# Kernel optimization log

Measured on AMD Instinct MI355X. Metric: run time of the kernel, lower is better.

Reference implementation:

```python
import jax, jax.numpy as jnp
import numpy as np

ALPHA = 0.2  # LeakyReLU negative slope
NEG_INF = jnp.float32(-9e15)


def gat_layer(h, mask, W, a, concat):
    """Dense GAT layer (pyGAT style). h: [B,N,Fin], mask: [N,N] bool, W: [Fin,Fout], a: [2*Fout,1]."""
    Wh = h @ W                                   # [B,N,Fout]
    F_out = W.shape[-1]
    e_src = Wh @ a[:F_out]                       # [B,N,1]
    e_dst = Wh @ a[F_out:]                       # [B,N,1]
    e = jax.nn.leaky_relu(e_src + jnp.swapaxes(e_dst, -1, -2), ALPHA)  # [B,N,N]
    att = jnp.where(mask, e, NEG_INF)
    att = jax.nn.softmax(att, axis=-1)
    out = att @ Wh                               # [B,N,Fout]
    return jax.nn.elu(out) if concat else out


def setup_inputs() -> dict:
    key = jax.random.key(0)
    ks = jax.random.split(key, 8)
    B, N, nfeat, nhid, nheads, emb, nclass = 4, 2048, 128, 64, 8, 64, 16
    slices = jax.random.normal(ks[0], (B, N, nfeat), jnp.float32)
    adj = jax.random.randint(ks[1], (N, N), 0, 2, jnp.int32)
    s = 1.0 / float(np.sqrt(nfeat))
    Ws = jax.random.uniform(ks[2], (nheads, nfeat, nhid), jnp.float32, -s, s)
    As = jax.random.uniform(ks[3], (nheads, 2 * nhid, 1), jnp.float32, -s, s)
    W1 = jax.random.uniform(ks[4], (nhid * nheads, emb), jnp.float32, -s, s)
    a1 = jax.random.uniform(ks[5], (2 * emb, 1), jnp.float32, -s, s)
    W2 = jax.random.uniform(ks[6], (emb, nclass), jnp.float32, -s, s)
    a2 = jax.random.uniform(ks[7], (2 * nclass, 1), jnp.float32, -s, s)
    return {"slices": slices, "adj": adj, "Ws": Ws, "As": As,
            "W1": W1, "a1": a1, "W2": W2, "a2": a2}


def reference(slices, adj, Ws, As, W1, a1, W2, a2):
    # Eval mode: dropout = 0 (identity).
    mask = adj > 0                               # [N,N], broadcasts over batch
    # Multi-head GAT with concat=True (ELU inside each head), vectorized over heads.
    heads = jax.vmap(lambda W, a: gat_layer(slices, mask, W, a, True))(Ws, As)  # [H,B,N,nhid]
    H, B, N, nh = heads.shape
    x = jnp.moveaxis(heads, 0, 2).reshape(B, N, H * nh)  # concat along features, head-major
    image_feature = jax.nn.elu(gat_layer(x, mask, W1, a1, False))              # [B,N,emb]
    pre = jax.nn.elu(gat_layer(image_feature, mask, W2, a2, False))            # [B,N,nclass]
    pre = pre[:, 0, :]                                                         # [B,nclass]
    return image_feature, pre
```

## Files before the change

### kernel.cpp

```cpp
#include <hip/hip_runtime.h>
#include <hip/hip_bf16.h>
#include <cstdint>


#define NN 2048

typedef float f32x4 __attribute__((ext_vector_type(4)));
typedef __bf16 bf16x8 __attribute__((ext_vector_type(8)));
typedef _Float16 f16;
typedef _Float16 f16x8 __attribute__((ext_vector_type(8)));

__device__ __forceinline__ void gll16(const void* g, void* l) {
  __builtin_amdgcn_global_load_lds(
      (const __attribute__((address_space(1))) unsigned int*)g,
      (__attribute__((address_space(3))) unsigned int*)l, 16, 0, 0);
}

__global__ __launch_bounds__(256) void prep_k(
    const int* __restrict__ adj, unsigned char* __restrict__ pm,
    const float* __restrict__ Ws, __bf16* __restrict__ WsFh, __bf16* __restrict__ WsFl,
    const float* __restrict__ W1, __bf16* __restrict__ W1Fh, __bf16* __restrict__ W1Fl) {
  const int bx = blockIdx.x, t = threadIdx.x;
  if (bx < 2048) {
    const int i = bx;
#pragma unroll
    for (int jt = 0; jt < 8; ++jt) {
      const int j = jt * 256 + t;
      pm[((long)(j >> 5) << 16) + i * 32 + (j & 31)] =
          adj[(long)i * NN + j] > 0 ? 0xFFu : 0u;
    }
  } else if (bx < 2304) {
    const int idx = (bx - 2048) * 256 + t;
    const int inst = idx >> 13;
    const int rem = idx & 8191;
    const int k = rem >> 6, n = rem & 63;
    const float v = Ws[(long)inst * 8192 + rem];
    const __bf16 vh = (__bf16)v;
    const int pos = ((k >> 5) * 4 + (n >> 4)) * 512 + (((k >> 3) & 3) * 16 + (n & 15)) * 8 + (k & 7);
    WsFh[(long)inst * 8192 + pos] = vh;
    WsFl[(long)inst * 8192 + pos] = (__bf16)(v - (float)vh);
  } else {
    const int idx = (bx - 2304) * 256 + t;
    const int k = idx >> 6, n = idx & 63;
    const float v = W1[idx];
    const __bf16 vh = (__bf16)v;
    const int pos = ((k >> 5) * 4 + (n >> 4)) * 512 + (((k >> 3) & 3) * 16 + (n & 15)) * 8 + (k & 7);
    W1Fh[pos] = vh;
    W1Fl[pos] = (__bf16)(v - (float)vh);
  }
}

struct GemmLd {
  float4 a0, a1;
  bf16x8 bh[4], bl[4];
};

__global__ __launch_bounds__(128) void gemm_mfma_k(
    const float* __restrict__ Aall, const __bf16* __restrict__ WFhi,
    const __bf16* __restrict__ WFlo, const float* __restrict__ avecAll,
    f16* __restrict__ WhBAll, float* __restrict__ Eo, float* __restrict__ Go,
    f16* __restrict__ Fo, f16* __restrict__ Ho, float* __restrict__ pC,
    int K, int KS, long aStrideB) {
  const int p = blockIdx.y;
  const int ks = blockIdx.z;
  const float* A = Aall + (long)(p & 3) * aStrideB;
  const long wfOff = (long)(p >> 2) * K * 64;
  const bf16x8* BhF = (const bf16x8*)(WFhi + wfOff);
  const bf16x8* BlF = (const bf16x8*)(WFlo + wfOff);

  const int t = threadIdx.x, lane = t & 63, wave = t >> 6;
  const int quad = lane >> 4, lm = lane & 15;
  const int i0w = blockIdx.x * 32 + wave * 16;
  const float* Arow = A + (long)(i0w + lm) * K;
  const int kBeg = ks * (K / KS), kEnd = kBeg + K / KS;

  f32x4 acc[4];
#pragma unroll
  for (int nt = 0; nt < 4; ++nt) acc[nt] = (f32x4){0.f, 0.f, 0.f, 0.f};

  auto LOAD = [&](GemmLd& L, int k0) {
    L.a0 = *(const float4*)(Arow + k0 + quad * 8);
    L.a1 = *(const float4*)(Arow + k0 + quad * 8 + 4);
    const int bbase = (k0 >> 5) * 256 + lane;
#pragma unroll
    for (int nt = 0; nt < 4; ++nt) {
      L.bh[nt] = BhF[bbase + nt * 64];
      L.bl[nt] = BlF[bbase + nt * 64];
    }
  };
  auto STEP = [&](const GemmLd& L) {
    const float av8[8] = {L.a0.x, L.a0.y, L.a0.z, L.a0.w, L.a1.x, L.a1.y, L.a1.z, L.a1.w};
    bf16x8 ah, al;
#pragma unroll
    for (int j = 0; j < 8; ++j) {
      const __bf16 h = (__bf16)av8[j];
      ah[j] = h;
      al[j] = (__bf16)(av8[j] - (float)h);
    }
#pragma unroll
    for (int nt = 0; nt < 4; ++nt) {
      acc[nt] = __builtin_amdgcn_mfma_f32_16x16x32_bf16(ah, L.bh[nt], acc[nt], 0, 0, 0);
      acc[nt] = __builtin_amdgcn_mfma_f32_16x16x32_bf16(al, L.bh[nt], acc[nt], 0, 0, 0);
      acc[nt] = __builtin_amdgcn_mfma_f32_16x16x32_bf16(ah, L.bl[nt], acc[nt], 0, 0, 0);
    }
  };

  GemmLd La, Lb;
  LOAD(La, kBeg);
  for (int k0 = kBeg; k0 < kEnd; k0 += 64) {
    LOAD(Lb, k0 + 32);
    STEP(La);
    LOAD(La, (k0 + 64 < kEnd) ? k0 + 64 : kBeg);
    STEP(Lb);
  }

  if (KS > 1) {
    float* pc = pC + ((long)(p * KS + ks) * NN) * 64;
#pragma unroll
    for (int reg = 0; reg < 4; ++reg) {
      const int row = i0w + quad * 4 + reg;
#pragma unroll
      for (int nt = 0; nt < 4; ++nt) pc[(long)row * 64 + nt * 16 + lm] = acc[nt][reg];
    }
    return;
  }

  const float* av = avecAll + (long)(p >> 2) * 128;
  f16* WhB = WhBAll + (long)p * NN * 64;
  float* E = Eo + (long)p * NN;
  float* G = Go + (long)p * NN;
  f16* F = Fo + (long)p * NN;
  f16* Hh = Ho + (long)p * NN;

  float alo[4], ahi[4];
#pragma unroll
  for (int nt = 0; nt < 4; ++nt) {
    alo[nt] = av[nt * 16 + lm];
    ahi[nt] = av[64 + nt * 16 + lm];
  }
#pragma unroll
  for (int reg = 0; reg < 4; ++reg) {
    float es = 0.f, ed = 0.f;
#pragma unroll
    for (int nt = 0; nt < 4; ++nt) {
      es += acc[nt][reg] * alo[nt];
      ed += acc[nt][reg] * ahi[nt];
    }
#pragma unroll
    for (int m = 1; m < 16; m <<= 1) {
      es += __shfl_xor(es, m);
      ed += __shfl_xor(ed, m);
    }
    if (lm == 0) {
      const int r = i0w + quad * 4 + reg;
      E[r] = __expf(es);
      G[r] = __expf(0.2f * es);
      F[r] = (f16)__expf(ed);
      Hh[r] = (f16)__expf(0.2f * ed);
    }
  }

  const int r0 = i0w + quad * 4;
  const long base = ((long)(r0 >> 5) * 4) * 512 + (((r0 >> 3) & 3) * 16 + lm) * 8 + (r0 & 7);
#pragma unroll
  for (int nt = 0; nt < 4; ++nt) {
    union { f16 h[4]; uint2 u; } pk;
#pragma unroll
    for (int q = 0; q < 4; ++q) pk.h[q] = (f16)acc[nt][q];
    *(uint2*)(WhB + base + nt * 512) = pk.u;
  }
}

__global__ __launch_bounds__(256) void gemm_epi_k(
    const float* __restrict__ pC, const float* __restrict__ avec,
    f16* __restrict__ WhBAll, float* __restrict__ Eo, float* __restrict__ Go,
    f16* __restrict__ Fo, f16* __restrict__ Ho, int KS) {
  const int inst = blockIdx.y;
  const int t = threadIdx.x;
  const int row = blockIdx.x * 16 + (t >> 4);
  const int cg = t & 15;
  f32x4 c = (f32x4){0.f, 0.f, 0.f, 0.f};
  for (int ks = 0; ks < KS; ++ks)
    c += *(const f32x4*)(pC + (((long)(inst * KS + ks) * NN) + row) * 64 + cg * 4);
  float es = 0.f, ed = 0.f;
#pragma unroll
  for (int q = 0; q < 4; ++q) {
    const int n = cg * 4 + q;
    es += c[q] * avec[n];
    ed += c[q] * avec[64 + n];
  }
#pragma unroll
  for (int m = 1; m < 16; m <<= 1) {
    es += __shfl_xor(es, m);
    ed += __shfl_xor(ed, m);
  }
  if (cg == 0) {
    Eo[(long)inst * NN + row] = __expf(es);
    Go[(long)inst * NN + row] = __expf(0.2f * es);
    Fo[(long)inst * NN + row] = (f16)__expf(ed);
    Ho[(long)inst * NN + row] = (f16)__expf(0.2f * ed);
  }
  f16* WhB = WhBAll + (long)inst * NN * 64;
#pragma unroll
  for (int q = 0; q < 4; ++q) {
    const int n = cg * 4 + q;
    const int pos = ((row >> 5) * 4 + (n >> 4)) * 512 + (((row >> 3) & 3) * 16 + (n & 15)) * 8 + (row & 7);
    WhB[pos] = (f16)c[q];
  }
}

__global__ __launch_bounds__(512) void attn_k(
    const f16* __restrict__ WhBAll, const float* __restrict__ Eb,
    const float* __restrict__ Gb, const f16* __restrict__ Fb,
    const f16* __restrict__ Hb, const unsigned char* __restrict__ pm,
    float* __restrict__ out1, int rowStride, long strideB,
    int jsCount, float* __restrict__ partAcc, float* __restrict__ partSum) {
  const int p = blockIdx.z;
  const int js = blockIdx.y;
  const f16* WhB = WhBAll + (long)p * NN * 64;
  const float* E = Eb + (long)p * NN;
  const float* G = Gb + (long)p * NN;
  const f16* F = Fb + (long)p * NN;
  const f16* Hv = Hb + (long)p * NN;
  const int t = threadIdx.x, lane = t & 63, wave = t >> 6;
  const int rw = wave & 3, half = wave >> 2;
  const int quad = lane >> 4, lm = lane & 15;
  const int i0 = blockIdx.x * 128;
  const int rbase = rw * 32;
  const int span = 64 / jsCount;
  const int nIter = span / 2;
  const int nStep = nIter / 2;
  const int kbBeg = js * span + half * nIter;

  __shared__ __align__(16) char pool[40960];
  f16* Fs = (f16*)pool;
  f16* Hs = (f16*)(pool + 4096);
  char* ring = pool + 8192 + half * 16384;

  const int r0g = i0 + rbase + lm, r1g = i0 + rbase + 16 + lm;
  const f16 e0 = (f16)E[r0g], g0 = (f16)G[r0g];
  const f16 e1 = (f16)E[r1g], g1 = (f16)G[r1g];
  f16x8 e0v, g0v, e1v, g1v;
#pragma unroll
  for (int j = 0; j < 8; ++j) { e0v[j] = e0; g0v[j] = g0; e1v[j] = e1; g1v[j] = g1; }

  f16x8 ones;
#pragma unroll
  for (int j = 0; j < 8; ++j) ones[j] = (lm == 0) ? (f16)1.0f : (f16)0.0f;

  if (wave == 0) {
#pragma unroll
    for (int c = 0; c < 4; ++c) gll16((const char*)F + c * 1024 + lane * 16, pool + c * 1024);
  } else if (wave == 1) {
#pragma unroll
    for (int c = 0; c < 4; ++c) gll16((const char*)Hv + c * 1024 + lane * 16, pool + 4096 + c * 1024);
  }
  if (rw == 0) {
    const char* gB = (const char*)WhB + (long)kbBeg * 4096;
#pragma unroll
    for (int c = 0; c < 8; ++c) gll16(gB + c * 1024 + lane * 16, ring + c * 1024);
  }
  __syncthreads();

  f32x4 acc0[4], acc1[4], sum0, sum1;
#pragma unroll
  for (int nt = 0; nt < 4; ++nt) {
    acc0[nt] = (f32x4){0.f, 0.f, 0.f, 0.f};
    acc1[nt] = (f32x4){0.f, 0.f, 0.f, 0.f};
  }
  sum0 = (f32x4){0.f, 0.f, 0.f, 0.f};
  sum1 = (f32x4){0.f, 0.f, 0.f, 0.f};

  const unsigned char* mp0 = pm + (long)(i0 + rbase + lm) * 32 + quad * 8;
  const unsigned char* mp1 = pm + (long)(i0 + rbase + 16 + lm) * 32 + quad * 8;

  for (int s = 0; s < nStep; ++s) {
    if (rw == 0 && s + 1 < nStep) {
      char* dst = ring + ((s + 1) & 1) * 8192;
      const char* gB = (const char*)WhB + (long)(kbBeg + (s + 1) * 2) * 4096;
#pragma unroll
      for (int c = 0; c < 8; ++c) gll16(gB + c * 1024 + lane * 16, dst + c * 1024);
    }
    const char* slot = ring + (s & 1) * 8192;
#pragma unroll
    for (int u = 0; u < 2; ++u) {
      const int kb = kbBeg + s * 2 + u;
      const char* bt = slot + u * 4096;
      const uint2 m0 = *(const uint2*)(mp0 + ((long)kb << 16));
      const uint2 m1 = *(const uint2*)(mp1 + ((long)kb << 16));
      const f16x8 F8 = *(const f16x8*)(Fs + kb * 32 + quad * 8);
      const f16x8 H8 = *(const f16x8*)(Hs + kb * 32 + quad * 8);

      union { f16x8 v; uint4 u4; } A0, A1;
      A0.v = __builtin_elementwise_max(e0v * F8, g0v * H8);
      A1.v = __builtin_elementwise_max(e1v * F8, g1v * H8);
      A0.u4.x &= __builtin_amdgcn_perm(0u, m0.x, 0x01010000u);
      A0.u4.y &= __builtin_amdgcn_perm(0u, m0.x, 0x03030202u);
      A0.u4.z &= __builtin_amdgcn_perm(0u, m0.y, 0x01010000u);
      A0.u4.w &= __builtin_amdgcn_perm(0u, m0.y, 0x03030202u);
      A1.u4.x &= __builtin_amdgcn_perm(0u, m1.x, 0x01010000u);
      A1.u4.y &= __builtin_amdgcn_perm(0u, m1.x, 0x03030202u);
      A1.u4.z &= __builtin_amdgcn_perm(0u, m1.y, 0x01010000u);
      A1.u4.w &= __builtin_amdgcn_perm(0u, m1.y, 0x03030202u);

#pragma unroll
      for (int nt = 0; nt < 4; ++nt) {
        const f16x8 bfr = *(const f16x8*)(bt + (nt * 64 + lane) * 16);
        acc0[nt] = __builtin_amdgcn_mfma_f32_16x16x32_f16(A0.v, bfr, acc0[nt], 0, 0, 0);
        acc1[nt] = __builtin_amdgcn_mfma_f32_16x16x32_f16(A1.v, bfr, acc1[nt], 0, 0, 0);
      }
      sum0 = __builtin_amdgcn_mfma_f32_16x16x32_f16(A0.v, ones, sum0, 0, 0, 0);
      sum1 = __builtin_amdgcn_mfma_f32_16x16x32_f16(A1.v, ones, sum1, 0, 0, 0);
    }
    __syncthreads();
  }

  float* cmb = (float*)pool;
  if (half == 1) {
    float* dst = &cmb[(rw * 64 + lane) * 40];
#pragma unroll
    for (int nt = 0; nt < 4; ++nt) {
      *(f32x4*)(dst + nt * 4) = acc0[nt];
      *(f32x4*)(dst + 16 + nt * 4) = acc1[nt];
    }
    *(f32x4*)(dst + 32) = sum0;
    *(f32x4*)(dst + 36) = sum1;
  }
  __syncthreads();
  if (half == 1) return;
  {
    const float* src = &cmb[(rw * 64 + lane) * 40];
#pragma unroll
    for (int nt = 0; nt < 4; ++nt) {
      acc0[nt] += *(const f32x4*)(src + nt * 4);
      acc1[nt] += *(const f32x4*)(src + 16 + nt * 4);
    }
    sum0 += *(const f32x4*)(src + 32);
    sum1 += *(const f32x4*)(src + 36);
  }

  if (jsCount == 1) {
#pragma unroll
    for (int g = 0; g < 2; ++g) {
      const f32x4* acc = g ? acc1 : acc0;
      const f32x4 sm = g ? sum1 : sum0;
#pragma unroll
      for (int reg = 0; reg < 4; ++reg) {
        const int row = i0 + rbase + g * 16 + quad * 4 + reg;
        const float ls = __shfl(sm[reg], quad * 16);
        const float il = ls > 0.f ? 1.f / ls : 0.f;
#pragma unroll
        for (int nt = 0; nt < 4; ++nt) {
          float v = acc[nt][reg] * il;
          v = v > 0.f ? v : expm1f(v);
          const long o = (long)(p & 3) * strideB + (long)row * rowStride + (p >> 2) * 64 + nt * 16 + lm;
          out1[o] = v;
        }
      }
    }
  } else {
    float* pAcc = partAcc + ((long)p * jsCount + js) * NN * 64;
    float* pSum = partSum + ((long)p * jsCount + js) * NN;
#pragma unroll
    for (int g = 0; g < 2; ++g) {
      const f32x4* acc = g ? acc1 : acc0;
      const f32x4 sm = g ? sum1 : sum0;
#pragma unroll
      for (int reg = 0; reg < 4; ++reg) {
        const int row = i0 + rbase + g * 16 + quad * 4 + reg;
#pragma unroll
        for (int nt = 0; nt < 4; ++nt) pAcc[(long)row * 64 + nt * 16 + lm] = acc[nt][reg];
        if (lm == 0) pSum[row] = sm[reg];
      }
    }
  }
}

__global__ __launch_bounds__(256) void combine_k(const float* __restrict__ partAcc,
                                                 const float* __restrict__ partSum,
                                                 float* __restrict__ img,
                                                 float* __restrict__ out, int JS) {
  const long idx = (long)blockIdx.x * 256 + threadIdx.x;
  const int cg = idx & 15;
  const int row = (int)((idx >> 4) & (NN - 1));
  const int inst = (int)(idx >> 15);
  f32x4 v = (f32x4){0.f, 0.f, 0.f, 0.f};
  float s = 0.f;
  for (int js = 0; js < JS; ++js) {
    const long b = ((long)inst * JS + js) * NN;
    v += *(const f32x4*)(partAcc + (b + row) * 64 + cg * 4);
    s += partSum[b + row];
  }
  const float il = s > 0.f ? 1.f / s : 0.f;
  f32x4 r;
#pragma unroll
  for (int q = 0; q < 4; ++q) {
    float x = v[q] * il;
    r[q] = x > 0.f ? x : expm1f(x);
  }
  const long o = ((long)inst * NN + row) * 64 + cg * 4;
  *(f32x4*)(img + o) = r;
  *(f32x4*)(out + o) = r;
}

__global__ __launch_bounds__(256) void layer3a_k(
    const float* __restrict__ img, const float* __restrict__ W2,
    const float* __restrict__ a2, const unsigned char* __restrict__ pm,
    float* __restrict__ pOut ) {
  const int bb = blockIdx.x, chunk = blockIdx.y, t = threadIdx.x;
  const float* A = img + (long)bb * NN * 64;
  __shared__ float w2alo[64], w2ahi[64];
  __shared__ float W2s[64][17];
  __shared__ float redc[4][17];
  if (t < 64) {
    float sl = 0.f, sh = 0.f;
#pragma unroll
    for (int c = 0; c < 16; ++c) {
      const float wv = W2[t * 16 + c];
      W2s[t][c] = wv;
      sl += wv * a2[c];
      sh += wv * a2[16 + c];
    }
    w2alo[t] = sl;
    w2ahi[t] = sh;
  }
  __syncthreads();

  float es = 0.f;
#pragma unroll 16
  for (int k = 0; k < 64; ++k) es += A[k] * w2alo[k];

  const int j = chunk * 256 + t;
  float arow[64];
#pragma unroll
  for (int q = 0; q < 16; ++q) *(f32x4*)(arow + q * 4) = *(const f32x4*)(A + (long)j * 64 + q * 4);
  float ed = 0.f;
#pragma unroll
  for (int k = 0; k < 64; ++k) ed += arow[k] * w2ahi[k];
  float e = es + ed;
  e = fmaxf(e, 0.2f * e);
  const float pv = pm[((long)(j >> 5) << 16) + (j & 31)] ? __expf(e) : 0.f;

  float acc[16];
#pragma unroll
  for (int c = 0; c < 16; ++c) {
    float wh = 0.f;
#pragma unroll
    for (int k = 0; k < 64; ++k) wh += arow[k] * W2s[k][c];
    acc[c] = pv * wh;
  }
  float lsum = pv;

#pragma unroll
  for (int off = 32; off > 0; off >>= 1) {
    lsum += __shfl_down(lsum, off);
#pragma unroll
    for (int c = 0; c < 16; ++c) acc[c] += __shfl_down(acc[c], off);
  }
  if ((t & 63) == 0) {
    const int wv = t >> 6;
#pragma unroll
    for (int c = 0; c < 16; ++c) redc[wv][c] = acc[c];
    redc[wv][16] = lsum;
  }
  __syncthreads();
  if (t < 17) {
    pOut[((long)bb * 8 + chunk) * 17 + t] =
        redc[0][t] + redc[1][t] + redc[2][t] + redc[3][t];
  }
}

__global__ __launch_bounds__(64) void layer3b_k(const float* __restrict__ pOut,
                                                float* __restrict__ outPre) {
  const int t = threadIdx.x;
  if (t >= 64) return;
  const int bb = t >> 4, c = t & 15;
  float a = 0.f, l = 0.f;
#pragma unroll
  for (int ch = 0; ch < 8; ++ch) {
    a += pOut[((long)bb * 8 + ch) * 17 + c];
    l += pOut[((long)bb * 8 + ch) * 17 + 16];
  }
  float v = a / l;
  v = v > 0.f ? v : expm1f(v);
  outPre[bb * 16 + c] = v;
}

extern "C" void kernel_launch(void* const* d_in, const int* in_sizes, int n_in,
                              void* d_out, int out_size, void* d_ws, size_t ws_size,
                              hipStream_t stream) {
  (void)in_sizes; (void)n_in; (void)out_size; (void)ws_size;
  constexpr int B = 4, N = NN, JS2 = 4, KS2 = 4;

  const float* slices = (const float*)d_in[0];
  const int* adj = (const int*)d_in[1];
  const float* Ws = (const float*)d_in[2];
  const float* As = (const float*)d_in[3];
  const float* W1 = (const float*)d_in[4];
  const float* a1 = (const float*)d_in[5];
  const float* W2 = (const float*)d_in[6];
  const float* a2 = (const float*)d_in[7];
  float* out = (float*)d_out;

  char* w = (char*)d_ws;
  size_t off = 0;
  auto alloc = [&](size_t bytes) {
    void* ptr = w + off;
    off += (bytes + 255) & ~(size_t)255;
    return ptr;
  };
  unsigned char* pm = (unsigned char*)alloc((size_t)64 * 65536);
  __bf16* WsFh = (__bf16*)alloc((size_t)8 * 128 * 64 * 2);
  __bf16* WsFl = (__bf16*)alloc((size_t)8 * 128 * 64 * 2);
  __bf16* W1Fh = (__bf16*)alloc((size_t)512 * 64 * 2);
  __bf16* W1Fl = (__bf16*)alloc((size_t)512 * 64 * 2);
  f16* WhB1 = (f16*)alloc((size_t)32 * N * 64 * 2);
  float* E1 = (float*)alloc((size_t)32 * N * 4);
  float* G1 = (float*)alloc((size_t)32 * N * 4);
  f16* F1 = (f16*)alloc((size_t)32 * N * 2);
  f16* H1 = (f16*)alloc((size_t)32 * N * 2);
  float* x = (float*)alloc((size_t)B * N * 512 * 4);
  float* pC2 = (float*)alloc((size_t)B * KS2 * N * 64 * 4);
  f16* WhB2 = (f16*)alloc((size_t)B * N * 64 * 2);
  float* E2 = (float*)alloc((size_t)B * N * 4);
  float* G2 = (float*)alloc((size_t)B * N * 4);
  f16* F2 = (f16*)alloc((size_t)B * N * 2);
  f16* H2 = (f16*)alloc((size_t)B * N * 2);
  float* img = (float*)alloc((size_t)B * N * 64 * 4);
  float* pAcc2 = (float*)alloc((size_t)B * JS2 * N * 64 * 4);
  float* pSum2 = (float*)alloc((size_t)B * JS2 * N * 4);
  float* pL3 = (float*)alloc((size_t)B * 8 * 17 * 4);

  prep_k<<<dim3(2432), dim3(256), 0, stream>>>(adj, pm, Ws, WsFh, WsFl, W1, W1Fh, W1Fl);

  gemm_mfma_k<<<dim3(N / 32, 32, 1), dim3(128), 0, stream>>>(
      slices, WsFh, WsFl, As, WhB1, E1, G1, F1, H1, (float*)nullptr,
      128, 1, (long)N * 128);
  attn_k<<<dim3(N / 128, 1, 32), dim3(512), 0, stream>>>(
      WhB1, E1, G1, F1, H1, pm, x, 512, (long)N * 512,
      1, (float*)nullptr, (float*)nullptr);

  gemm_mfma_k<<<dim3(N / 32, 4, KS2), dim3(128), 0, stream>>>(
      x, W1Fh, W1Fl, a1, (f16*)nullptr, (float*)nullptr, (float*)nullptr,
      (f16*)nullptr, (f16*)nullptr, pC2, 512, KS2, (long)N * 512);
  gemm_epi_k<<<dim3(N / 16, 4), dim3(256), 0, stream>>>(
      pC2, a1, WhB2, E2, G2, F2, H2, KS2);
  attn_k<<<dim3(N / 128, JS2, 4), dim3(512), 0, stream>>>(
      WhB2, E2, G2, F2, H2, pm, (float*)nullptr, 64, (long)N * 64,
      JS2, pAcc2, pSum2);
  combine_k<<<dim3(B * N * 16 / 256), dim3(256), 0, stream>>>(pAcc2, pSum2, img, out, JS2);

  layer3a_k<<<dim3(B, 8), dim3(256), 0, stream>>>(img, W2, a2, pm, pL3);
  layer3b_k<<<dim3(1), dim3(64), 0, stream>>>(pL3, out + (size_t)B * N * 64);
}
```

Before: 162.3 us.

## Fuse split-K GEMM reduction, enlarge attention tiles, merge layer-3 kernels via ticket

The second-layer split-K GEMM and its separate epilogue kernel are replaced by a single 512-thread kernel that reduces the four K slices in shared memory. The attention kernel now gives each wave 64 rows instead of 32 and drops the LDS ring and global_load_lds staging in favour of direct register double-buffered loads. The two layer-3 kernels are merged using an atomic ticket, so the last block does the final combine. The aim is fewer launches and less global round-trip traffic, at the cost of more register pressure in attention and the loss of LDS sharing of B tiles.

```diff
diff --git a/kernel.cpp b/kernel.cpp
--- a/kernel.cpp
+++ b/kernel.cpp
@@ -10,17 +10,13 @@
 typedef _Float16 f16;
 typedef _Float16 f16x8 __attribute__((ext_vector_type(8)));
 
-__device__ __forceinline__ void gll16(const void* g, void* l) {
-  __builtin_amdgcn_global_load_lds(
-      (const __attribute__((address_space(1))) unsigned int*)g,
-      (__attribute__((address_space(3))) unsigned int*)l, 16, 0, 0);
-}
-
 __global__ __launch_bounds__(256) void prep_k(
     const int* __restrict__ adj, unsigned char* __restrict__ pm,
     const float* __restrict__ Ws, __bf16* __restrict__ WsFh, __bf16* __restrict__ WsFl,
-    const float* __restrict__ W1, __bf16* __restrict__ W1Fh, __bf16* __restrict__ W1Fl) {
+    const float* __restrict__ W1, __bf16* __restrict__ W1Fh, __bf16* __restrict__ W1Fl,
+    unsigned int* __restrict__ ticket) {
   const int bx = blockIdx.x, t = threadIdx.x;
+  if (bx == 0 && t == 0) *ticket = 0u;
   if (bx < 2048) {
     const int i = bx;
 #pragma unroll
@@ -59,10 +55,9 @@
     const float* __restrict__ Aall, const __bf16* __restrict__ WFhi,
     const __bf16* __restrict__ WFlo, const float* __restrict__ avecAll,
     f16* __restrict__ WhBAll, float* __restrict__ Eo, float* __restrict__ Go,
-    f16* __restrict__ Fo, f16* __restrict__ Ho, float* __restrict__ pC,
-    int K, int KS, long aStrideB) {
+    f16* __restrict__ Fo, f16* __restrict__ Ho,
+    int K, long aStrideB) {
   const int p = blockIdx.y;
-  const int ks = blockIdx.z;
   const float* A = Aall + (long)(p & 3) * aStrideB;
   const long wfOff = (long)(p >> 2) * K * 64;
   const bf16x8* BhF = (const bf16x8*)(WFhi + wfOff);
@@ -72,7 +67,7 @@
   const int quad = lane >> 4, lm = lane & 15;
   const int i0w = blockIdx.x * 32 + wave * 16;
   const float* Arow = A + (long)(i0w + lm) * K;
-  const int kBeg = ks * (K / KS), kEnd = kBeg + K / KS;
+  const int kBeg = 0, kEnd = K;
 
   f32x4 acc[4];
 #pragma unroll
@@ -114,17 +109,6 @@
     STEP(Lb);
   }
 
-  if (KS > 1) {
-    float* pc = pC + ((long)(p * KS + ks) * NN) * 64;
-#pragma unroll
-    for (int reg = 0; reg < 4; ++reg) {
-      const int row = i0w + quad * 4 + reg;
-#pragma unroll
-      for (int nt = 0; nt < 4; ++nt) pc[(long)row * 64 + nt * 16 + lm] = acc[nt][reg];
-    }
-    return;
-  }
-
   const float* av = avecAll + (long)(p >> 2) * 128;
   f16* WhB = WhBAll + (long)p * NN * 64;
   float* E = Eo + (long)p * NN;
@@ -171,43 +155,110 @@
   }
 }
 
-__global__ __launch_bounds__(256) void gemm_epi_k(
-    const float* __restrict__ pC, const float* __restrict__ avec,
+__global__ __launch_bounds__(512) void gemm2_k(
+    const float* __restrict__ Aall, const __bf16* __restrict__ WFhi,
+    const __bf16* __restrict__ WFlo, const float* __restrict__ avec,
     f16* __restrict__ WhBAll, float* __restrict__ Eo, float* __restrict__ Go,
-    f16* __restrict__ Fo, f16* __restrict__ Ho, int KS) {
-  const int inst = blockIdx.y;
-  const int t = threadIdx.x;
-  const int row = blockIdx.x * 16 + (t >> 4);
-  const int cg = t & 15;
-  f32x4 c = (f32x4){0.f, 0.f, 0.f, 0.f};
-  for (int ks = 0; ks < KS; ++ks)
-    c += *(const f32x4*)(pC + (((long)(inst * KS + ks) * NN) + row) * 64 + cg * 4);
-  float es = 0.f, ed = 0.f;
-#pragma unroll
-  for (int q = 0; q < 4; ++q) {
-    const int n = cg * 4 + q;
-    es += c[q] * avec[n];
-    ed += c[q] * avec[64 + n];
-  }
-#pragma unroll
-  for (int m = 1; m < 16; m <<= 1) {
-    es += __shfl_xor(es, m);
-    ed += __shfl_xor(ed, m);
-  }
-  if (cg == 0) {
-    Eo[(long)inst * NN + row] = __expf(es);
-    Go[(long)inst * NN + row] = __expf(0.2f * es);
-    Fo[(long)inst * NN + row] = (f16)__expf(ed);
-    Ho[(long)inst * NN + row] = (f16)__expf(0.2f * ed);
-  }
-  f16* WhB = WhBAll + (long)inst * NN * 64;
-#pragma unroll
-  for (int q = 0; q < 4; ++q) {
-    const int n = cg * 4 + q;
-    const int pos = ((row >> 5) * 4 + (n >> 4)) * 512 + (((row >> 3) & 3) * 16 + (n & 15)) * 8 + (row & 7);
-    WhB[pos] = (f16)c[q];
-  }
-}
+    f16* __restrict__ Fo, f16* __restrict__ Ho) {
+  const int p = blockIdx.y;
+  const float* A = Aall + (long)p * NN * 512;
+  const bf16x8* BhF = (const bf16x8*)WFhi;
+  const bf16x8* BlF = (const bf16x8*)WFlo;
+  const int t = threadIdx.x, lane = t & 63, wave = t >> 6;
+  const int ks = wave & 3, rh = wave >> 2;
+  const int quad = lane >> 4, lm = lane & 15;
+  const int i0 = blockIdx.x * 32;
+  const float* Arow = A + (long)(i0 + rh * 16 + lm) * 512;
+  const int kBeg = ks * 128, kEnd = kBeg + 128;
+
+  f32x4 acc[4];
+#pragma unroll
+  for (int nt = 0; nt < 4; ++nt) acc[nt] = (f32x4){0.f, 0.f, 0.f, 0.f};
+
+  auto LOAD = [&](GemmLd& L, int k0) {
+    L.a0 = *(const float4*)(Arow + k0 + quad * 8);
+    L.a1 = *(const float4*)(Arow + k0 + quad * 8 + 4);
+    const int bbase = (k0 >> 5) * 256 + lane;
+#pragma unroll
+    for (int nt = 0; nt < 4; ++nt) {
+      L.bh[nt] = BhF[bbase + nt * 64];
+      L.bl[nt] = BlF[bbase + nt * 64];
+    }
+  };
+  auto STEP = [&](const GemmLd& L) {
+    const float av8[8] = {L.a0.x, L.a0.y, L.a0.z, L.a0.w, L.a1.x, L.a1.y, L.a1.z, L.a1.w};
+    bf16x8 ah, al;
+#pragma unroll
+    for (int j = 0; j < 8; ++j) {
+      const __bf16 h = (__bf16)av8[j];
+      ah[j] = h;
+      al[j] = (__bf16)(av8[j] - (float)h);
+    }
+#pragma unroll
+    for (int nt = 0; nt < 4; ++nt) {
+      acc[nt] = __builtin_amdgcn_mfma_f32_16x16x32_bf16(ah, L.bh[nt], acc[nt], 0, 0, 0);
+      acc[nt] = __builtin_amdgcn_mfma_f32_16x16x32_bf16(al, L.bh[nt], acc[nt], 0, 0, 0);
+      acc[nt] = __builtin_amdgcn_mfma_f32_16x16x32_bf16(ah, L.bl[nt], acc[nt], 0, 0, 0);
+    }
+  };
+
+  GemmLd La, Lb;
+  LOAD(La, kBeg);
+  for (int k0 = kBeg; k0 < kEnd; k0 += 64) {
+    LOAD(Lb, k0 + 32);
+    STEP(La);
+    LOAD(La, (k0 + 64 < kEnd) ? k0 + 64 : kBeg);
+    STEP(Lb);
+  }
+
+  __shared__ __align__(16) float red[8][4][64][4];
+#pragma unroll
+  for (int nt = 0; nt < 4; ++nt) *(f32x4*)&red[wave][nt][lane][0] = acc[nt];
+  __syncthreads();
+
+  const int n = lane, rgrp = wave;
+  const int rh2 = rgrp >> 2, q2 = rgrp & 3;
+  const int ln = q2 * 16 + (n & 15), ntq = n >> 4;
+  f32x4 c4 = *(const f32x4*)&red[rh2 * 4 + 0][ntq][ln][0];
+#pragma unroll
+  for (int ksum = 1; ksum < 4; ++ksum)
+    c4 += *(const f32x4*)&red[rh2 * 4 + ksum][ntq][ln][0];
+
+  f32x4 es4 = c4 * avec[n];
+  f32x4 ed4 = c4 * avec[64 + n];
+#pragma unroll
+  for (int m = 1; m < 64; m <<= 1) {
+#pragma unroll
+    for (int q = 0; q < 4; ++q) {
+      es4[q] += __shfl_xor(es4[q], m);
+      ed4[q] += __shfl_xor(ed4[q], m);
+    }
+  }
+  const int row0 = i0 + rgrp * 4;
+  if (n == 0) {
+#pragma unroll
+    for (int reg = 0; reg < 4; ++reg) {
+      const int row = row0 + reg;
+      Eo[(long)p * NN + row] = __expf(es4[reg]);
+      Go[(long)p * NN + row] = __expf(0.2f * es4[reg]);
+      Fo[(long)p * NN + row] = (f16)__expf(ed4[reg]);
+      Ho[(long)p * NN + row] = (f16)__expf(0.2f * ed4[reg]);
+    }
+  }
+  f16* WhB = WhBAll + (long)p * NN * 64;
+  union { f16 h[4]; uint2 u; } pk;
+#pragma unroll
+  for (int reg = 0; reg < 4; ++reg) pk.h[reg] = (f16)c4[reg];
+  const long pos = ((long)(row0 >> 5) * 4 + ntq) * 512 +
+                   ((((row0 >> 3) & 3) * 16 + (n & 15)) * 8) + (row0 & 7);
+  *(uint2*)(WhB + pos) = pk.u;
+}
+
+struct KbLd {
+  f16x8 F8, H8;
+  f16x8 b[4];
+  uint2 m[4];
+};
 
 __global__ __launch_bounds__(512) void attn_k(
     const f16* __restrict__ WhBAll, const float* __restrict__ Eb,
@@ -220,138 +271,115 @@
   const f16* WhB = WhBAll + (long)p * NN * 64;
   const float* E = Eb + (long)p * NN;
   const float* G = Gb + (long)p * NN;
-  const f16* F = Fb + (long)p * NN;
-  const f16* Hv = Hb + (long)p * NN;
+  const f16* Fg = Fb + (long)p * NN;
+  const f16* Hg = Hb + (long)p * NN;
   const int t = threadIdx.x, lane = t & 63, wave = t >> 6;
   const int rw = wave & 3, half = wave >> 2;
   const int quad = lane >> 4, lm = lane & 15;
-  const int i0 = blockIdx.x * 128;
-  const int rbase = rw * 32;
+  const int i0 = blockIdx.x * 256;
+  const int rbase = rw * 64;
   const int span = 64 / jsCount;
   const int nIter = span / 2;
-  const int nStep = nIter / 2;
-  const int kbBeg = js * span + half * nIter;
-
-  __shared__ __align__(16) char pool[40960];
-  f16* Fs = (f16*)pool;
-  f16* Hs = (f16*)(pool + 4096);
-  char* ring = pool + 8192 + half * 16384;
-
-  const int r0g = i0 + rbase + lm, r1g = i0 + rbase + 16 + lm;
-  const f16 e0 = (f16)E[r0g], g0 = (f16)G[r0g];
-  const f16 e1 = (f16)E[r1g], g1 = (f16)G[r1g];
-  f16x8 e0v, g0v, e1v, g1v;
-#pragma unroll
-  for (int j = 0; j < 8; ++j) { e0v[j] = e0; g0v[j] = g0; e1v[j] = e1; g1v[j] = g1; }
+  const int kbBeg = js * span + half * nIter, kbEnd = kbBeg + nIter;
+
+  __shared__ __align__(16) float cmb[20480];
+
+  f16x8 ev[4], gv[4];
+#pragma unroll
+  for (int g = 0; g < 4; ++g) {
+    const int r = i0 + rbase + g * 16 + lm;
+    const f16 e = (f16)E[r], gg = (f16)G[r];
+#pragma unroll
+    for (int j = 0; j < 8; ++j) { ev[g][j] = e; gv[g][j] = gg; }
+  }
 
   f16x8 ones;
 #pragma unroll
   for (int j = 0; j < 8; ++j) ones[j] = (lm == 0) ? (f16)1.0f : (f16)0.0f;
 
-  if (wave == 0) {
-#pragma unroll
-    for (int c = 0; c < 4; ++c) gll16((const char*)F + c * 1024 + lane * 16, pool + c * 1024);
-  } else if (wave == 1) {
-#pragma unroll
-    for (int c = 0; c < 4; ++c) gll16((const char*)Hv + c * 1024 + lane * 16, pool + 4096 + c * 1024);
-  }
-  if (rw == 0) {
-    const char* gB = (const char*)WhB + (long)kbBeg * 4096;
-#pragma unroll
-    for (int c = 0; c < 8; ++c) gll16(gB + c * 1024 + lane * 16, ring + c * 1024);
-  }
-  __syncthreads();
-
-  f32x4 acc0[4], acc1[4], sum0, sum1;
-#pragma unroll
-  for (int nt = 0; nt < 4; ++nt) {
-    acc0[nt] = (f32x4){0.f, 0.f, 0.f, 0.f};
-    acc1[nt] = (f32x4){0.f, 0.f, 0.f, 0.f};
-  }
-  sum0 = (f32x4){0.f, 0.f, 0.f, 0.f};
-  sum1 = (f32x4){0.f, 0.f, 0.f, 0.f};
-
-  const unsigned char* mp0 = pm + (long)(i0 + rbase + lm) * 32 + quad * 8;
-  const unsigned char* mp1 = pm + (long)(i0 + rbase + 16 + lm) * 32 + quad * 8;
-
-  for (int s = 0; s < nStep; ++s) {
-    if (rw == 0 && s + 1 < nStep) {
-      char* dst = ring + ((s + 1) & 1) * 8192;
-      const char* gB = (const char*)WhB + (long)(kbBeg + (s + 1) * 2) * 4096;
-#pragma unroll
-      for (int c = 0; c < 8; ++c) gll16(gB + c * 1024 + lane * 16, dst + c * 1024);
-    }
-    const char* slot = ring + (s & 1) * 8192;
-#pragma unroll
-    for (int u = 0; u < 2; ++u) {
-      const int kb = kbBeg + s * 2 + u;
-      const char* bt = slot + u * 4096;
-      const uint2 m0 = *(const uint2*)(mp0 + ((long)kb << 16));
-      const uint2 m1 = *(const uint2*)(mp1 + ((long)kb << 16));
-      const f16x8 F8 = *(const f16x8*)(Fs + kb * 32 + quad * 8);
-      const f16x8 H8 = *(const f16x8*)(Hs + kb * 32 + quad * 8);
-
-      union { f16x8 v; uint4 u4; } A0, A1;
-      A0.v = __builtin_elementwise_max(e0v * F8, g0v * H8);
-      A1.v = __builtin_elementwise_max(e1v * F8, g1v * H8);
-      A0.u4.x &= __builtin_amdgcn_perm(0u, m0.x, 0x01010000u);
-      A0.u4.y &= __builtin_amdgcn_perm(0u, m0.x, 0x03030202u);
-      A0.u4.z &= __builtin_amdgcn_perm(0u, m0.y, 0x01010000u);
-      A0.u4.w &= __builtin_amdgcn_perm(0u, m0.y, 0x03030202u);
-      A1.u4.x &= __builtin_amdgcn_perm(0u, m1.x, 0x01010000u);
-      A1.u4.y &= __builtin_amdgcn_perm(0u, m1.x, 0x03030202u);
-      A1.u4.z &= __builtin_amdgcn_perm(0u, m1.y, 0x01010000u);
-      A1.u4.w &= __builtin_amdgcn_perm(0u, m1.y, 0x03030202u);
-
-#pragma unroll
-      for (int nt = 0; nt < 4; ++nt) {
-        const f16x8 bfr = *(const f16x8*)(bt + (nt * 64 + lane) * 16);
-        acc0[nt] = __builtin_amdgcn_mfma_f32_16x16x32_f16(A0.v, bfr, acc0[nt], 0, 0, 0);
-        acc1[nt] = __builtin_amdgcn_mfma_f32_16x16x32_f16(A1.v, bfr, acc1[nt], 0, 0, 0);
-      }
-      sum0 = __builtin_amdgcn_mfma_f32_16x16x32_f16(A0.v, ones, sum0, 0, 0, 0);
-      sum1 = __builtin_amdgcn_mfma_f32_16x16x32_f16(A1.v, ones, sum1, 0, 0, 0);
-    }
-    __syncthreads();
-  }
-
-  float* cmb = (float*)pool;
+  f32x4 acc[4][4], sum[4];
+#pragma unroll
+  for (int g = 0; g < 4; ++g) {
+    sum[g] = (f32x4){0.f, 0.f, 0.f, 0.f};
+#pragma unroll
+    for (int nt = 0; nt < 4; ++nt) acc[g][nt] = (f32x4){0.f, 0.f, 0.f, 0.f};
+  }
+
+  const unsigned char* mp[4];
+#pragma unroll
+  for (int g = 0; g < 4; ++g)
+    mp[g] = pm + (long)(i0 + rbase + g * 16 + lm) * 32 + quad * 8;
+
+  auto LD = [&](KbLd& L, int kb) {
+    L.F8 = *(const f16x8*)(Fg + kb * 32 + quad * 8);
+    L.H8 = *(const f16x8*)(Hg + kb * 32 + quad * 8);
+#pragma unroll
+    for (int nt = 0; nt < 4; ++nt)
+      L.b[nt] = *(const f16x8*)(WhB + (long)kb * 2048 + (nt * 64 + lane) * 8);
+#pragma unroll
+    for (int g = 0; g < 4; ++g)
+      L.m[g] = *(const uint2*)(mp[g] + ((long)kb << 16));
+  };
+  auto CP = [&](const KbLd& L) {
+    union { f16x8 v; uint4 u4; } A[4];
+#pragma unroll
+    for (int g = 0; g < 4; ++g) {
+      A[g].v = __builtin_elementwise_max(ev[g] * L.F8, gv[g] * L.H8);
+      A[g].u4.x &= __builtin_amdgcn_perm(0u, L.m[g].x, 0x01010000u);
+      A[g].u4.y &= __builtin_amdgcn_perm(0u, L.m[g].x, 0x03030202u);
+      A[g].u4.z &= __builtin_amdgcn_perm(0u, L.m[g].y, 0x01010000u);
+      A[g].u4.w &= __builtin_amdgcn_perm(0u, L.m[g].y, 0x03030202u);
+    }
+#pragma unroll
+    for (int nt = 0; nt < 4; ++nt) {
+#pragma unroll
+      for (int g = 0; g < 4; ++g)
+        acc[g][nt] = __builtin_amdgcn_mfma_f32_16x16x32_f16(A[g].v, L.b[nt], acc[g][nt], 0, 0, 0);
+    }
+#pragma unroll
+    for (int g = 0; g < 4; ++g)
+      sum[g] = __builtin_amdgcn_mfma_f32_16x16x32_f16(A[g].v, ones, sum[g], 0, 0, 0);
+  };
+
+  KbLd La, Lb2;
+  LD(La, kbBeg);
+  for (int kb = kbBeg; kb < kbEnd; kb += 2) {
+    LD(Lb2, kb + 1);
+    CP(La);
+    if (kb + 2 < kbEnd) LD(La, kb + 2);
+    CP(Lb2);
+  }
+
   if (half == 1) {
-    float* dst = &cmb[(rw * 64 + lane) * 40];
-#pragma unroll
-    for (int nt = 0; nt < 4; ++nt) {
-      *(f32x4*)(dst + nt * 4) = acc0[nt];
-      *(f32x4*)(dst + 16 + nt * 4) = acc1[nt];
-    }
-    *(f32x4*)(dst + 32) = sum0;
-    *(f32x4*)(dst + 36) = sum1;
+#pragma unroll
+    for (int g = 0; g < 4; ++g) {
+#pragma unroll
+      for (int nt = 0; nt < 4; ++nt)
+        *(f32x4*)&cmb[((rw * 20 + g * 4 + nt) * 64 + lane) * 4] = acc[g][nt];
+      *(f32x4*)&cmb[((rw * 20 + 16 + g) * 64 + lane) * 4] = sum[g];
+    }
   }
   __syncthreads();
   if (half == 1) return;
-  {
-    const float* src = &cmb[(rw * 64 + lane) * 40];
-#pragma unroll
-    for (int nt = 0; nt < 4; ++nt) {
-      acc0[nt] += *(const f32x4*)(src + nt * 4);
-      acc1[nt] += *(const f32x4*)(src + 16 + nt * 4);
-    }
-    sum0 += *(const f32x4*)(src + 32);
-    sum1 += *(const f32x4*)(src + 36);
+#pragma unroll
+  for (int g = 0; g < 4; ++g) {
+#pragma unroll
+    for (int nt = 0; nt < 4; ++nt)
+      acc[g][nt] += *(const f32x4*)&cmb[((rw * 20 + g * 4 + nt) * 64 + lane) * 4];
+    sum[g] += *(const f32x4*)&cmb[((rw * 20 + 16 + g) * 64 + lane) * 4];
   }
 
   if (jsCount == 1) {
 #pragma unroll
-    for (int g = 0; g < 2; ++g) {
-      const f32x4* acc = g ? acc1 : acc0;
-      const f32x4 sm = g ? sum1 : sum0;
+    for (int g = 0; g < 4; ++g) {
 #pragma unroll
       for (int reg = 0; reg < 4; ++reg) {
         const int row = i0 + rbase + g * 16 + quad * 4 + reg;
-        const float ls = __shfl(sm[reg], quad * 16);
+        const float ls = __shfl(sum[g][reg], quad * 16);
         const float il = ls > 0.f ? 1.f / ls : 0.f;
 #pragma unroll
         for (int nt = 0; nt < 4; ++nt) {
-          float v = acc[nt][reg] * il;
+          float v = acc[g][nt][reg] * il;
           v = v > 0.f ? v : expm1f(v);
           const long o = (long)(p & 3) * strideB + (long)row * rowStride + (p >> 2) * 64 + nt * 16 + lm;
           out1[o] = v;
@@ -362,15 +390,13 @@
     float* pAcc = partAcc + ((long)p * jsCount + js) * NN * 64;
     float* pSum = partSum + ((long)p * jsCount + js) * NN;
 #pragma unroll
-    for (int g = 0; g < 2; ++g) {
-      const f32x4* acc = g ? acc1 : acc0;
-      const f32x4 sm = g ? sum1 : sum0;
+    for (int g = 0; g < 4; ++g) {
 #pragma unroll
       for (int reg = 0; reg < 4; ++reg) {
         const int row = i0 + rbase + g * 16 + quad * 4 + reg;
 #pragma unroll
-        for (int nt = 0; nt < 4; ++nt) pAcc[(long)row * 64 + nt * 16 + lm] = acc[nt][reg];
-        if (lm == 0) pSum[row] = sm[reg];
+        for (int nt = 0; nt < 4; ++nt) pAcc[(long)row * 64 + nt * 16 + lm] = acc[g][nt][reg];
+        if (lm == 0) pSum[row] = sum[g][reg];
       }
     }
   }
@@ -406,12 +432,14 @@
 __global__ __launch_bounds__(256) void layer3a_k(
     const float* __restrict__ img, const float* __restrict__ W2,
     const float* __restrict__ a2, const unsigned char* __restrict__ pm,
-    float* __restrict__ pOut ) {
+    float* __restrict__ pOut , float* __restrict__ outPre,
+    unsigned int* __restrict__ ticket) {
   const int bb = blockIdx.x, chunk = blockIdx.y, t = threadIdx.x;
   const float* A = img + (long)bb * NN * 64;
   __shared__ float w2alo[64], w2ahi[64];
   __shared__ float W2s[64][17];
   __shared__ float redc[4][17];
+  __shared__ int lastS;
   if (t < 64) {
     float sl = 0.f, sh = 0.f;
 #pragma unroll
@@ -465,32 +493,36 @@
   }
   __syncthreads();
   if (t < 17) {
-    pOut[((long)bb * 8 + chunk) * 17 + t] =
-        redc[0][t] + redc[1][t] + redc[2][t] + redc[3][t];
-  }
-}
-
-__global__ __launch_bounds__(64) void layer3b_k(const float* __restrict__ pOut,
-                                                float* __restrict__ outPre) {
-  const int t = threadIdx.x;
-  if (t >= 64) return;
-  const int bb = t >> 4, c = t & 15;
-  float a = 0.f, l = 0.f;
-#pragma unroll
-  for (int ch = 0; ch < 8; ++ch) {
-    a += pOut[((long)bb * 8 + ch) * 17 + c];
-    l += pOut[((long)bb * 8 + ch) * 17 + 16];
-  }
-  float v = a / l;
-  v = v > 0.f ? v : expm1f(v);
-  outPre[bb * 16 + c] = v;
+    __hip_atomic_store(&pOut[((long)bb * 8 + chunk) * 17 + t],
+                       redc[0][t] + redc[1][t] + redc[2][t] + redc[3][t],
+                       __ATOMIC_RELAXED, __HIP_MEMORY_SCOPE_AGENT);
+  }
+  __syncthreads();
+  if (t == 0)
+    lastS = (__hip_atomic_fetch_add(ticket, 1u, __ATOMIC_ACQ_REL,
+                                    __HIP_MEMORY_SCOPE_AGENT) == 31u);
+  __syncthreads();
+  if (lastS && t < 64) {
+    const int b2 = t >> 4, c2 = t & 15;
+    float a = 0.f, l = 0.f;
+#pragma unroll
+    for (int ch = 0; ch < 8; ++ch) {
+      a += __hip_atomic_load(&pOut[((long)b2 * 8 + ch) * 17 + c2],
+                             __ATOMIC_RELAXED, __HIP_MEMORY_SCOPE_AGENT);
+      l += __hip_atomic_load(&pOut[((long)b2 * 8 + ch) * 17 + 16],
+                             __ATOMIC_RELAXED, __HIP_MEMORY_SCOPE_AGENT);
+    }
+    float v = a / l;
+    v = v > 0.f ? v : expm1f(v);
+    outPre[b2 * 16 + c2] = v;
+  }
 }
 
 extern "C" void kernel_launch(void* const* d_in, const int* in_sizes, int n_in,
                               void* d_out, int out_size, void* d_ws, size_t ws_size,
                               hipStream_t stream) {
   (void)in_sizes; (void)n_in; (void)out_size; (void)ws_size;
-  constexpr int B = 4, N = NN, JS2 = 4, KS2 = 4;
+  constexpr int B = 4, N = NN, JS2 = 4;
 
   const float* slices = (const float*)d_in[0];
   const int* adj = (const int*)d_in[1];
@@ -520,7 +552,6 @@
   f16* F1 = (f16*)alloc((size_t)32 * N * 2);
   f16* H1 = (f16*)alloc((size_t)32 * N * 2);
   float* x = (float*)alloc((size_t)B * N * 512 * 4);
-  float* pC2 = (float*)alloc((size_t)B * KS2 * N * 64 * 4);
   f16* WhB2 = (f16*)alloc((size_t)B * N * 64 * 2);
   float* E2 = (float*)alloc((size_t)B * N * 4);
   float* G2 = (float*)alloc((size_t)B * N * 4);
@@ -530,26 +561,23 @@
   float* pAcc2 = (float*)alloc((size_t)B * JS2 * N * 64 * 4);
   float* pSum2 = (float*)alloc((size_t)B * JS2 * N * 4);
   float* pL3 = (float*)alloc((size_t)B * 8 * 17 * 4);
-
-  prep_k<<<dim3(2432), dim3(256), 0, stream>>>(adj, pm, Ws, WsFh, WsFl, W1, W1Fh, W1Fl);
-
-  gemm_mfma_k<<<dim3(N / 32, 32, 1), dim3(128), 0, stream>>>(
-      slices, WsFh, WsFl, As, WhB1, E1, G1, F1, H1, (float*)nullptr,
-      128, 1, (long)N * 128);
-  attn_k<<<dim3(N / 128, 1, 32), dim3(512), 0, stream>>>(
+  unsigned int* ticket = (unsigned int*)alloc(256);
+
+  prep_k<<<dim3(2432), dim3(256), 0, stream>>>(adj, pm, Ws, WsFh, WsFl, W1, W1Fh, W1Fl, ticket);
+
+  gemm_mfma_k<<<dim3(N / 32, 32), dim3(128), 0, stream>>>(
+      slices, WsFh, WsFl, As, WhB1, E1, G1, F1, H1, 128, (long)N * 128);
+  attn_k<<<dim3(N / 256, 1, 32), dim3(512), 0, stream>>>(
       WhB1, E1, G1, F1, H1, pm, x, 512, (long)N * 512,
       1, (float*)nullptr, (float*)nullptr);
 
-  gemm_mfma_k<<<dim3(N / 32, 4, KS2), dim3(128), 0, stream>>>(
-      x, W1Fh, W1Fl, a1, (f16*)nullptr, (float*)nullptr, (float*)nullptr,
-      (f16*)nullptr, (f16*)nullptr, pC2, 512, KS2, (long)N * 512);
-  gemm_epi_k<<<dim3(N / 16, 4), dim3(256), 0, stream>>>(
-      pC2, a1, WhB2, E2, G2, F2, H2, KS2);
-  attn_k<<<dim3(N / 128, JS2, 4), dim3(512), 0, stream>>>(
+  gemm2_k<<<dim3(N / 32, 4), dim3(512), 0, stream>>>(
+      x, W1Fh, W1Fl, a1, WhB2, E2, G2, F2, H2);
+  attn_k<<<dim3(N / 256, JS2, 4), dim3(512), 0, stream>>>(
       WhB2, E2, G2, F2, H2, pm, (float*)nullptr, 64, (long)N * 64,
       JS2, pAcc2, pSum2);
   combine_k<<<dim3(B * N * 16 / 256), dim3(256), 0, stream>>>(pAcc2, pSum2, img, out, JS2);
 
-  layer3a_k<<<dim3(B, 8), dim3(256), 0, stream>>>(img, W2, a2, pm, pL3);
-  layer3b_k<<<dim3(1), dim3(64), 0, stream>>>(pL3, out + (size_t)B * N * 64);
-}
+  layer3a_k<<<dim3(B, 8), dim3(256), 0, stream>>>(img, W2, a2, pm, pL3,
+                                                  out + (size_t)B * N * 64, ticket);
+}
```

Measured after the change: 163.2 us. About the same (+0.6%).
